# Performance work log

Hardware: AMD Instinct MI355X
Metric: run time of the kernel (lower is better)

Reference implementation:

```python
import jax, jax.numpy as jnp
import numpy as np
import math

B, S, D, H, DFF = 2, 2048, 1024, 16, 4096
DK = D // H
EPS = 1e-5

def layer_norm(x, g, b):
    mu = jnp.mean(x, axis=-1, keepdims=True)
    var = jnp.mean(jnp.square(x - mu), axis=-1, keepdims=True)
    return (x - mu) * jax.lax.rsqrt(var + EPS) * g + b

def setup_inputs() -> dict:
    key = jax.random.key(0)
    ks = jax.random.split(key, 12)
    p = lambda k, shape: (jax.random.normal(k, shape, jnp.float32) * 0.02)
    return {
        "x": jax.random.normal(ks[0], (B, S, D), jnp.float32),
        "mask": jax.random.randint(ks[1], (B, S, S), 0, 2).astype(bool),
        "Wq": p(ks[2], (D, D)), "bq": jnp.zeros((D,), jnp.float32),
        "Wk": p(ks[3], (D, D)), "bk": jnp.zeros((D,), jnp.float32),
        "Wv": p(ks[4], (D, D)), "bv": jnp.zeros((D,), jnp.float32),
        "Wo": p(ks[5], (D, D)), "bo": jnp.zeros((D,), jnp.float32),
        "W1": p(ks[6], (DFF, D)), "b1": jnp.zeros((DFF,), jnp.float32),
        "W2": p(ks[7], (D, DFF)), "b2": jnp.zeros((D,), jnp.float32),
        "g_attn": jnp.ones((D,), jnp.float32), "b_attn": jnp.zeros((D,), jnp.float32),
        "g_ffn": jnp.ones((D,), jnp.float32), "b_ffn": jnp.zeros((D,), jnp.float32),
    }

def reference(x, mask, Wq, bq, Wk, bk, Wv, bv, Wo, bo, W1, b1, W2, b2, g_attn, b_attn, g_ffn, b_ffn):
    orig_dtype = x.dtype
    nx = layer_norm(x, g_attn, b_attn)
    # project and split heads: [B,S,D] -> [B,H,S,DK]
    split = lambda t: t.reshape(B, S, H, DK).transpose(0, 2, 1, 3)
    q = split(nx @ Wq.T + bq)
    k = split(nx @ Wk.T + bk)
    v = split(nx @ Wv.T + bv)
    # explicit fp32 upcast as in the original
    scores = jnp.einsum('bhqd,bhkd->bhqk', q.astype(jnp.float32), k.astype(jnp.float32)) / math.sqrt(DK)
    scores = jnp.where(mask[:, None, :, :], jnp.float32(-10000.0), scores)
    attn = jax.nn.softmax(scores, axis=-1)
    context = jnp.einsum('bhqk,bhkd->bhqd', attn, v.astype(jnp.float32)).astype(orig_dtype)
    context = context.transpose(0, 2, 1, 3).reshape(B, S, D)
    x = x + (context @ Wo.T + bo)
    nx = layer_norm(x, g_ffn, b_ffn)
    h = jax.nn.gelu(nx @ W1.T + b1, approximate=False)  # torch F.gelu default is exact erf
    x = x + (h @ W2.T + b2)
    return x
```

## Files before the change

kernel.cpp:

```cpp
#include <hip/hip_runtime.h>
#include <stdint.h>

#define B_ 2
#define S_ 2048
#define D_ 1024
#define H_ 16
#define DK_ 64
#define DFF_ 4096
#define M_ (B_*S_)

typedef __bf16 bf16x8 __attribute__((ext_vector_type(8)));
typedef float  f32x4  __attribute__((ext_vector_type(4)));

__device__ __forceinline__ unsigned short f2bf(float f) {
    union { float f; unsigned int u; } x; x.f = f;
    unsigned int r = x.u + 0x7FFFu + ((x.u >> 16) & 1u);
    return (unsigned short)(r >> 16);
}
__device__ __forceinline__ float bf2f(unsigned short h) {
    union { unsigned int u; float f; } x; x.u = ((unsigned int)h) << 16;
    return x.f;
}

__device__ __forceinline__ void gl16(const void* g, void* l) {
    __builtin_amdgcn_global_load_lds((const __attribute__((address_space(1))) unsigned int*)g,
                                     (__attribute__((address_space(3))) unsigned int*)l, 16, 0, 0);
}

static constexpr size_t OFS_XC   = 256;
static constexpr size_t OFS_MASK = OFS_XC   + 8388608;
static constexpr size_t OFS_WQKV = OFS_MASK + 8388608;
static constexpr size_t OFS_WO   = OFS_WQKV + 6291456;
static constexpr size_t OFS_W1   = OFS_WO   + 2097152;
static constexpr size_t OFS_W2   = OFS_W1   + 8388608;
static constexpr size_t OFS_BIAS = OFS_W2   + 8388608;
static constexpr size_t OFS_S0   = OFS_BIAS + 53248;
static constexpr size_t OFS_S1   = OFS_S0   + 8388608;
static constexpr size_t OFS_S2   = OFS_S1   + 8388608;
static constexpr size_t OFS_S3   = OFS_S2   + 8388608;
static constexpr size_t OFS_H    = OFS_S3   + 8388608;

#define BOF_QKV 0
#define BOF_O   3072
#define BOF_2   4096
#define BOF_GA  5120
#define BOF_BA  6144
#define BOF_GF  7168
#define BOF_BF  8192
#define BOF_1   9216

__global__ void detect_kernel(const unsigned int* __restrict__ g_attn,
                              const unsigned int* __restrict__ mask,
                              int* __restrict__ flags) {
    const int u = threadIdx.x;
    unsigned int w0 = mask[u], w1 = mask[64 + u];
    bool a32  = (w0 <= 1u) && (w1 <= 1u);
    bool af32 = ((w0 == 0u) || (w0 == 0x3F800000u)) && ((w1 == 0u) || (w1 == 0x3F800000u));
    bool a8 = true;
    #pragma unroll
    for (int j = 0; j < 4; j++)
        a8 = a8 && (((w0 >> (8*j)) & 0xFFu) <= 1u) && (((w1 >> (8*j)) & 0xFFu) <= 1u);
    int all32 = __all(a32), all8 = __all(a8), allf32 = __all(af32);
    if (u == 0) {
        unsigned int g0 = g_attn[0];
        int fm = (g0 == 0x3F800000u) ? 0 : ((g0 == 0x3C003C00u) ? 2 : 1);
        int mm = all32 ? 0 : (all8 ? 1 : (allf32 ? 2 : 3));
        flags[0] = fm; flags[1] = mm;
    }
}

struct BigSrc { const void* s[7]; };

__device__ __forceinline__ void conv4(const void* src, size_t si,
                                      unsigned short* dst, size_t di, int fm) {
    ushort4 ov;
    if (fm == 1) {
        ov = *(const ushort4*)((const unsigned short*)src + si);
    } else if (fm == 0) {
        const float* fp = (const float*)src + si;
        float4 f = *(const float4*)fp;
        ov.x = f2bf(f.x); ov.y = f2bf(f.y); ov.z = f2bf(f.z); ov.w = f2bf(f.w);
    } else {
        const _Float16* hp = (const _Float16*)src + si;
        ov.x = f2bf((float)hp[0]); ov.y = f2bf((float)hp[1]);
        ov.z = f2bf((float)hp[2]); ov.w = f2bf((float)hp[3]);
    }
    *(ushort4*)(dst + di) = ov;
}

__global__ __launch_bounds__(256) void convert_big_kernel(BigSrc srcs, char* ws) {
    const int fm = ((const int*)ws)[0];
    size_t i = ((size_t)blockIdx.x * 256 + threadIdx.x) * 4;
    if (i >= 16777216) return;
    if (i < 4194304) {
        conv4(srcs.s[0], i, (unsigned short*)(ws + OFS_XC), i, fm);
    } else if (i < 7340032) {
        size_t off = i - 4194304;
        int sub = (int)(off >> 20);
        size_t loc = off & 1048575;
        conv4(srcs.s[1 + sub], loc, (unsigned short*)(ws + OFS_WQKV), off, fm);
    } else if (i < 8388608) {
        size_t off = i - 7340032;
        conv4(srcs.s[4], off, (unsigned short*)(ws + OFS_WO), off, fm);
    } else if (i < 12582912) {
        size_t off = i - 8388608;
        conv4(srcs.s[5], off, (unsigned short*)(ws + OFS_W1), off, fm);
    } else {
        size_t off = i - 12582912;
        conv4(srcs.s[6], off, (unsigned short*)(ws + OFS_W2), off, fm);
    }
}

struct SmallSrc { const void* s[10]; };

__global__ __launch_bounds__(256) void convert_small_kernel(SmallSrc srcs, char* ws) {
    int idx = blockIdx.x * 256 + threadIdx.x;
    if (idx >= 13312) return;
    const int fm = ((const int*)ws)[0];
    int seg = idx >> 10; if (seg > 9) seg = 9;
    int loc = idx - seg * 1024;
    const void* s = srcs.s[seg];
    float f;
    if (fm == 1)      f = bf2f(((const unsigned short*)s)[loc]);
    else if (fm == 0) f = ((const float*)s)[loc];
    else              f = (float)((const _Float16*)s)[loc];
    ((float*)(ws + OFS_BIAS))[idx] = f;
}

__global__ __launch_bounds__(256) void mask_bits_kernel(const void* msrc, char* ws) {
    const int mm = ((const int*)ws)[1];
    size_t e = (size_t)blockIdx.x * 256 + threadIdx.x;
    bool p;
    if (mm == 0)      p = ((const int*)msrc)[e] != 0;
    else if (mm == 1) p = ((const unsigned char*)msrc)[e] != 0;
    else if (mm == 2) p = ((const unsigned int*)msrc)[e] != 0;
    else              p = ((const unsigned short*)msrc)[e] != 0;
    unsigned long long bal = __ballot(p);
    if ((threadIdx.x & 63) == 0)
        ((unsigned long long*)(ws + OFS_MASK))[e >> 6] = bal;
}

template<int IN32>
__global__ __launch_bounds__(256) void ln_kernel(const void* __restrict__ xin,
                                                 const float* __restrict__ g,
                                                 const float* __restrict__ b,
                                                 unsigned short* __restrict__ out) {
    const int row = blockIdx.x;
    const int t = threadIdx.x;
    float f0, f1, f2, f3;
    if (IN32) {
        const float* xr = (const float*)xin + (size_t)row * D_;
        float4 xv = *(const float4*)(xr + t * 4);
        f0 = xv.x; f1 = xv.y; f2 = xv.z; f3 = xv.w;
    } else {
        const unsigned short* xr = (const unsigned short*)xin + (size_t)row * D_;
        ushort4 xv = *(const ushort4*)(xr + t * 4);
        f0 = bf2f(xv.x); f1 = bf2f(xv.y); f2 = bf2f(xv.z); f3 = bf2f(xv.w);
    }
    float s = f0 + f1 + f2 + f3;
    float q = f0*f0 + f1*f1 + f2*f2 + f3*f3;
    for (int m = 1; m < 64; m <<= 1) { s += __shfl_xor(s, m); q += __shfl_xor(q, m); }
    __shared__ float red[8];
    __shared__ float mv[2];
    int w = t >> 6, u = t & 63;
    if (u == 0) { red[w*2] = s; red[w*2+1] = q; }
    __syncthreads();
    if (t == 0) {
        float S = red[0] + red[2] + red[4] + red[6];
        float Q = red[1] + red[3] + red[5] + red[7];
        float mu = S * (1.0f / D_);
        float var = Q * (1.0f / D_) - mu * mu;
        mv[0] = mu; mv[1] = rsqrtf(var + 1e-5f);
    }
    __syncthreads();
    float mu = mv[0], r = mv[1];
    int i = t * 4;
    ushort4 ov;
    ov.x = f2bf((f0 - mu) * r * g[i]   + b[i]);
    ov.y = f2bf((f1 - mu) * r * g[i+1] + b[i+1]);
    ov.z = f2bf((f2 - mu) * r * g[i+2] + b[i+2]);
    ov.w = f2bf((f3 - mu) * r * g[i+3] + b[i+3]);
    *(ushort4*)(out + (size_t)row * D_ + i) = ov;
}

template<int EPI>
__global__ __launch_bounds__(256) void gemm_bt_kernel(
    const unsigned short* __restrict__ A,
    const unsigned short* __restrict__ Bm,
    const float* __restrict__ bias,
    void* __restrict__ out,
    float* __restrict__ p1,
    unsigned short* __restrict__ q_out,
    unsigned short* __restrict__ k_out,
    unsigned short* __restrict__ vT_out,
    int M, int N, int K, int Kstride)
{
    __shared__ __attribute__((aligned(16))) unsigned short ldsA[2][4096];
    __shared__ __attribute__((aligned(16))) unsigned short ldsB[2][4096];
    const int t = threadIdx.x;
    const int w = t >> 6, u = t & 63, quad = u >> 4, l15 = u & 15;
    const int bx = blockIdx.x, by = blockIdx.y;
    const int z = (EPI == 5) ? blockIdx.z : 0;

    const int c0 = t, c1 = t + 256;
    const int ar0 = by*128 + ((c0 >> 6) << 4) + (c0 & 15), ak0 = ((c0 >> 4) & 3) * 8;
    const int ar1 = by*128 + ((c1 >> 6) << 4) + (c1 & 15), ak1 = ((c1 >> 4) & 3) * 8;
    const int br0 = bx*128 + ((c0 >> 6) << 4) + (c0 & 15);
    const int br1 = bx*128 + ((c1 >> 6) << 4) + (c1 & 15);
    const size_t kofs = (size_t)z * K;
    const unsigned short* pa0 = A  + (size_t)ar0 * Kstride + kofs + ak0;
    const unsigned short* pa1 = A  + (size_t)ar1 * Kstride + kofs + ak1;
    const unsigned short* pb0 = Bm + (size_t)br0 * Kstride + kofs + ak0;
    const unsigned short* pb1 = Bm + (size_t)br1 * Kstride + kofs + ak1;

    const int cbase0 = (w * 64) * 8;
    const int cbase1 = (256 + w * 64) * 8;

    f32x4 acc[4][4];
    #pragma unroll
    for (int i = 0; i < 4; i++)
        #pragma unroll
        for (int j = 0; j < 4; j++) acc[i][j] = (f32x4){0.f, 0.f, 0.f, 0.f};

    const int mbase = (w >> 1) * 4;
    const int nbase = (w & 1) * 4;

    for (int k0 = 0; k0 < K; k0 += 64) {
        __syncthreads();
        gl16(pa0,      &ldsA[0][cbase0]);
        gl16(pa1,      &ldsA[0][cbase1]);
        gl16(pb0,      &ldsB[0][cbase0]);
        gl16(pb1,      &ldsB[0][cbase1]);
        gl16(pa0 + 32, &ldsA[1][cbase0]);
        gl16(pa1 + 32, &ldsA[1][cbase1]);
        gl16(pb0 + 32, &ldsB[1][cbase0]);
        gl16(pb1 + 32, &ldsB[1][cbase1]);
        pa0 += 64; pa1 += 64; pb0 += 64; pb1 += 64;
        __syncthreads();
        #pragma unroll
        for (int sub = 0; sub < 2; sub++) {
            bf16x8 af[4], bfr[4];
            #pragma unroll
            for (int mt = 0; mt < 4; mt++) af[mt]  = *(const bf16x8*)&ldsA[sub][((mbase+mt)*64 + u) * 8];
            #pragma unroll
            for (int nt = 0; nt < 4; nt++) bfr[nt] = *(const bf16x8*)&ldsB[sub][((nbase+nt)*64 + u) * 8];
            #pragma unroll
            for (int mt = 0; mt < 4; mt++)
                #pragma unroll
                for (int nt = 0; nt < 4; nt++)
                    acc[mt][nt] = __builtin_amdgcn_mfma_f32_16x16x32_bf16(af[mt], bfr[nt], acc[mt][nt], 0, 0, 0);
        }
    }

    #pragma unroll
    for (int mt = 0; mt < 4; mt++) {
        #pragma unroll
        for (int nt = 0; nt < 4; nt++) {
            const int m0 = by*128 + (w >> 1)*64 + mt*16 + quad*4;
            const int n  = bx*128 + (w & 1)*64 + nt*16 + l15;
            float bn = 0.f;
            if constexpr (EPI != 5) bn = bias[n];
            float val[4];
            #pragma unroll
            for (int r = 0; r < 4; r++) val[r] = acc[mt][nt][r] + bn;
            if constexpr (EPI == 1) {
                #pragma unroll
                for (int r = 0; r < 4; r++) {
                    float v = val[r];
                    float ge = 0.5f * v * (1.0f + erff(v * 0.70710678118654752f));
                    ((unsigned short*)out)[(size_t)(m0 + r) * N + n] = f2bf(ge);
                }
            } else if constexpr (EPI == 2) {
                int sel = n >> 10, nn = n & 1023;
                int hh = nn >> 6, dk = nn & 63;
                int bb = m0 >> 11, ss = m0 & 2047;
                if (sel < 2) {
                    unsigned short* dst = sel == 0 ? q_out : k_out;
                    #pragma unroll
                    for (int r = 0; r < 4; r++)
                        dst[(((size_t)bb * H_ + hh) * S_ + ss + r) * DK_ + dk] = f2bf(val[r]);
                } else {
                    ushort4 pk;
                    pk.x = f2bf(val[0]); pk.y = f2bf(val[1]);
                    pk.z = f2bf(val[2]); pk.w = f2bf(val[3]);
                    *(ushort4*)&vT_out[(((size_t)bb * H_ + hh) * DK_ + dk) * S_ + ss] = pk;
                }
            } else {
                float* dst = z ? p1 : (float*)out;
                #pragma unroll
                for (int r = 0; r < 4; r++)
                    dst[(size_t)(m0 + r) * N + n] = val[r];
            }
        }
    }
}

template<int EPI>
__global__ __launch_bounds__(512, 2) void gemm256_kernel(
    const unsigned short* __restrict__ A,
    const unsigned short* __restrict__ Bm,
    const float* __restrict__ bias,
    void* __restrict__ out,
    unsigned short* __restrict__ q_out,
    unsigned short* __restrict__ k_out,
    unsigned short* __restrict__ vT_out,
    int N)
{
    __shared__ __attribute__((aligned(16))) unsigned short sh[2][2][16384];
    const int t = threadIdx.x, w = t >> 6, u = t & 63, quad = u >> 4, l15 = u & 15;
    const int wm = w >> 2, wn = w & 3;
    const int bx = blockIdx.x, by = blockIdx.y;

    const int r1 = t >> 3, cc1 = t & 7, cs1 = cc1 ^ (r1 & 7);
    const unsigned short* srcA = A  + ((size_t)by * 256 + r1) * 1024 + cs1 * 8;
    const unsigned short* srcB = Bm + ((size_t)bx * 256 + r1) * 1024 + cs1 * 8;

    const int rowA = wm * 16 + l15;
    const int rowB = wn * 16 + l15;
    const int cx0 = ((quad    ) ^ (l15 & 7)) * 8;
    const int cx1 = ((quad + 4) ^ (l15 & 7)) * 8;

    f32x4 acc[8][4];
    #pragma unroll
    for (int i = 0; i < 8; i++)
        #pragma unroll
        for (int j = 0; j < 4; j++) acc[i][j] = (f32x4){0.f, 0.f, 0.f, 0.f};

#define STAGE(bufi, mat, half, tile) { \
    const unsigned short* _s = ((mat) ? srcB : srcA) + (size_t)(half) * 131072 + (size_t)(tile) * 64; \
    unsigned short* _d = &sh[bufi][mat][(half) * 8192 + w * 512]; \
    gl16(_s, _d); gl16(_s + 65536, _d + 4096); }

#define LOAD_A(bufi, mh) { \
    const unsigned short* _p = &sh[bufi][0][0]; \
    _Pragma("unroll") \
    for (int f = 0; f < 4; f++) { \
        aF[f][0] = *(const bf16x8*)&_p[((mh) * 128 + f * 32 + rowA) * 64 + cx0]; \
        aF[f][1] = *(const bf16x8*)&_p[((mh) * 128 + f * 32 + rowA) * 64 + cx1]; \
    } }

#define LOAD_B(bufi, nh) { \
    const unsigned short* _p = &sh[bufi][1][0]; \
    _Pragma("unroll") \
    for (int g = 0; g < 2; g++) { \
        bF[nh][g][0] = *(const bf16x8*)&_p[((nh) * 128 + g * 64 + rowB) * 64 + cx0]; \
        bF[nh][g][1] = *(const bf16x8*)&_p[((nh) * 128 + g * 64 + rowB) * 64 + cx1]; \
    } }

#define QUADC(mh, nh) \
    __builtin_amdgcn_s_setprio(1); \
    _Pragma("unroll") \
    for (int ks = 0; ks < 2; ks++) \
        _Pragma("unroll") \
        for (int f = 0; f < 4; f++) \
            _Pragma("unroll") \
            for (int g = 0; g < 2; g++) \
                acc[(mh)*4 + f][(nh)*2 + g] = __builtin_amdgcn_mfma_f32_16x16x32_bf16( \
                    aF[f][ks], bF[nh][g][ks], acc[(mh)*4 + f][(nh)*2 + g], 0, 0, 0); \
    __builtin_amdgcn_s_setprio(0);

#define BARR __builtin_amdgcn_s_barrier()
#define VM6  asm volatile("s_waitcnt vmcnt(6)" ::: "memory")

    STAGE(0, 0, 0, 0);
    STAGE(0, 1, 0, 0);
    STAGE(0, 0, 1, 0);
    STAGE(0, 1, 1, 0);
    STAGE(1, 0, 0, 1);
    STAGE(1, 1, 0, 1);
    STAGE(1, 0, 1, 1);
    VM6;
    BARR;

    bf16x8 aF[4][2];
    bf16x8 bF[2][2][2];

    #pragma unroll 1
    for (int it = 0; it < 8; ++it) {
        const int t1 = 2 * it + 1;
        const int t2 = (it < 7) ? 2 * it + 2 : 15;
        const int t3 = (it < 7) ? 2 * it + 3 : 15;

        LOAD_A(0, 0); LOAD_B(0, 0);
        STAGE(1, 1, 1, t1);
        BARR; QUADC(0, 0); BARR;
        LOAD_B(0, 1);
        STAGE(0, 0, 0, t2);
        BARR; QUADC(0, 1); BARR;
        LOAD_A(0, 1);
        STAGE(0, 1, 0, t2);
        BARR; QUADC(1, 0); BARR;
        STAGE(0, 0, 1, t2);
        VM6;
        BARR; QUADC(1, 1); BARR;
        LOAD_A(1, 0); LOAD_B(1, 0);
        STAGE(0, 1, 1, t2);
        BARR; QUADC(0, 0); BARR;
        LOAD_B(1, 1);
        STAGE(1, 0, 0, t3);
        BARR; QUADC(0, 1); BARR;
        LOAD_A(1, 1);
        STAGE(1, 1, 0, t3);
        BARR; QUADC(1, 0); BARR;
        STAGE(1, 0, 1, t3);
        VM6;
        BARR; QUADC(1, 1); BARR;
    }
    asm volatile("s_waitcnt vmcnt(0)" ::: "memory");

#undef STAGE
#undef LOAD_A
#undef LOAD_B
#undef QUADC
#undef BARR
#undef VM6

    if constexpr (EPI == 1) {
        #pragma unroll
        for (int f = 0; f < 8; f++) {
            #pragma unroll
            for (int g = 0; g < 4; g++) {
                const int m0 = by * 256 + f * 32 + wm * 16 + quad * 4;
                const int n  = bx * 256 + g * 64 + wn * 16 + l15;
                const float bn = bias[n];
                #pragma unroll
                for (int r = 0; r < 4; r++) {
                    float v = acc[f][g][r] + bn;
                    float ge = 0.5f * v * (1.0f + erff(v * 0.70710678118654752f));
                    ((unsigned short*)out)[(size_t)(m0 + r) * N + n] = f2bf(ge);
                }
            }
        }
    } else {
        const int sel = bx >> 2;
        #pragma unroll
        for (int f = 0; f < 8; f++) {
            #pragma unroll
            for (int g = 0; g < 4; g++) {
                const int m0 = by * 256 + f * 32 + wm * 16 + quad * 4;
                const int n  = bx * 256 + g * 64 + wn * 16 + l15;
                const float bn = bias[n];
                const int nn = n & 1023, hh = nn >> 6, dk = nn & 63;
                const int bb = m0 >> 11, ss = m0 & 2047;
                if (sel < 2) {
                    unsigned short* dst = sel == 0 ? q_out : k_out;
                    #pragma unroll
                    for (int r = 0; r < 4; r++)
                        dst[(((size_t)bb * H_ + hh) * S_ + ss + r) * DK_ + dk] = f2bf(acc[f][g][r] + bn);
                } else {
                    ushort4 pk;
                    pk.x = f2bf(acc[f][g][0] + bn); pk.y = f2bf(acc[f][g][1] + bn);
                    pk.z = f2bf(acc[f][g][2] + bn); pk.w = f2bf(acc[f][g][3] + bn);
                    *(ushort4*)&vT_out[(((size_t)bb * H_ + hh) * DK_ + dk) * S_ + ss] = pk;
                }
            }
        }
    }
}

template<int FINAL>
__global__ __launch_bounds__(256) void reduce_kernel(
    const float* __restrict__ p0, const float* __restrict__ p1,
    const float* __restrict__ bias, const void* __restrict__ res,
    void* __restrict__ out, const int* __restrict__ flags)
{
    size_t i = ((size_t)blockIdx.x * 256 + threadIdx.x) * 4;
    int n = (int)(i & 1023);
    float4 a = *(const float4*)(p0 + i);
    float4 b = *(const float4*)(p1 + i);
    const float4 bi = *(const float4*)(bias + n);
    float v0 = a.x + b.x + bi.x, v1 = a.y + b.y + bi.y;
    float v2 = a.z + b.z + bi.z, v3 = a.w + b.w + bi.w;
    if constexpr (FINAL == 0) {
        ushort4 rr = *(const ushort4*)((const unsigned short*)res + i);
        v0 += bf2f(rr.x); v1 += bf2f(rr.y); v2 += bf2f(rr.z); v3 += bf2f(rr.w);
        float4 ov = {v0, v1, v2, v3};
        *(float4*)((float*)out + i) = ov;
    } else {
        float4 rr = *(const float4*)((const float*)res + i);
        v0 += rr.x; v1 += rr.y; v2 += rr.z; v3 += rr.w;
        const int fm = flags[0];
        if (fm == 0) {
            float4 ov = {v0, v1, v2, v3};
            *(float4*)((float*)out + i) = ov;
        } else if (fm == 2) {
            _Float16* op = (_Float16*)out + i;
            op[0] = (_Float16)v0; op[1] = (_Float16)v1;
            op[2] = (_Float16)v2; op[3] = (_Float16)v3;
        } else {
            ushort4 ov;
            ov.x = f2bf(v0); ov.y = f2bf(v1); ov.z = f2bf(v2); ov.w = f2bf(v3);
            *(ushort4*)((unsigned short*)out + i) = ov;
        }
    }
}

__global__ __launch_bounds__(512) void attn_kernel(
    const unsigned short* __restrict__ q,
    const unsigned short* __restrict__ k,
    const unsigned short* __restrict__ vT,
    const unsigned long long* __restrict__ mb,
    unsigned short* __restrict__ ctx)
{
    const int blk = blockIdx.x;
    const int xcd = blk & 7;
    const int slot = blk >> 3;
    const int qt = slot & 15;
    const int pg = slot >> 4;
    const int p  = xcd + 8 * pg;
    const int h = p & 15, b = p >> 4;
    const int bh = b * H_ + h;

    const int t = threadIdx.x, w = t >> 6, u = t & 63, quad = u >> 4, l15 = u & 15;

    __shared__ __attribute__((aligned(16))) unsigned short Kt[512 * 8];
    __shared__ __attribute__((aligned(16))) unsigned short Vt[512 * 8];
    __shared__ __attribute__((aligned(16))) unsigned short Pw[8][16 * 72];

    const size_t base = (size_t)bh * S_ * DK_;
    const int qr0 = qt * 128 + w * 16;

    bf16x8 aq[2];
    #pragma unroll
    for (int hf = 0; hf < 2; hf++)
        aq[hf] = *(const bf16x8*)(q + base + (size_t)(qr0 + l15) * DK_ + hf*32 + quad*8);

    const int sr = t >> 3, sc = (t & 7) ^ (sr & 7);
    const unsigned short* kp = k  + base + (size_t)sr * DK_ + sc * 8;
    const unsigned short* vp = vT + base + (size_t)sr * S_  + sc * 8;
    unsigned short* lk = &Kt[(w * 64) * 8];
    unsigned short* lv = &Vt[(w * 64) * 8];

    f32x4 o[4];
    #pragma unroll
    for (int nt = 0; nt < 4; nt++) o[nt] = (f32x4){0.f, 0.f, 0.f, 0.f};
    float ls[4] = {0.f, 0.f, 0.f, 0.f};
    const float C = 0.125f * 1.4426950408889634f;

    for (int kt = 0; kt < S_ / 64; kt++) {
        unsigned long long m64[4];
        #pragma unroll
        for (int r = 0; r < 4; r++)
            m64[r] = mb[((size_t)b * S_ + qr0 + quad*4 + r) * 32 + kt];

        __syncthreads();
        gl16(kp, lk);
        gl16(vp, lv);
        kp += 64 * DK_;
        vp += 64;
        __syncthreads();

        f32x4 s4[4];
        #pragma unroll
        for (int nt = 0; nt < 4; nt++) s4[nt] = (f32x4){0.f, 0.f, 0.f, 0.f};
        #pragma unroll
        for (int nt = 0; nt < 4; nt++) {
            int rr = nt * 16 + l15;
            #pragma unroll
            for (int hf = 0; hf < 2; hf++) {
                int cc = (hf * 4 + quad) ^ (rr & 7);
                bf16x8 bk = *(const bf16x8*)&Kt[(rr * 8 + cc) * 8];
                s4[nt] = __builtin_amdgcn_mfma_f32_16x16x32_bf16(aq[hf], bk, s4[nt], 0, 0, 0);
            }
        }

        #pragma unroll
        for (int r = 0; r < 4; r++) {
            unsigned int lo = (unsigned int)m64[r], hi = (unsigned int)(m64[r] >> 32);
            #pragma unroll
            for (int nt = 0; nt < 4; nt++) {
                unsigned int word = (nt & 2) ? hi : lo;
                unsigned int bit = (word >> ((nt & 1) * 16 + l15)) & 1u;
                float arg = bit ? -20000.0f : s4[nt][r] * C;
                float e = exp2f(arg);
                ls[r] += e;
                Pw[w][(quad * 4 + r) * 72 + nt * 16 + l15] = f2bf(e);
            }
        }

        #pragma unroll
        for (int ks = 0; ks < 2; ks++) {
            bf16x8 ap = *(const bf16x8*)&Pw[w][l15 * 72 + ks * 32 + quad * 8];
            #pragma unroll
            for (int nt = 0; nt < 4; nt++) {
                int rr = nt * 16 + l15;
                int cc = (ks * 4 + quad) ^ (rr & 7);
                bf16x8 bv = *(const bf16x8*)&Vt[(rr * 8 + cc) * 8];
                o[nt] = __builtin_amdgcn_mfma_f32_16x16x32_bf16(ap, bv, o[nt], 0, 0, 0);
            }
        }
    }

    #pragma unroll
    for (int r = 0; r < 4; r++) {
        float l = ls[r];
        l += __shfl_xor(l, 1); l += __shfl_xor(l, 2);
        l += __shfl_xor(l, 4); l += __shfl_xor(l, 8);
        float inv = 1.0f / l;
        int qg = qr0 + quad * 4 + r;
        #pragma unroll
        for (int nt = 0; nt < 4; nt++)
            ctx[((size_t)b * S_ + qg) * D_ + h * DK_ + nt * 16 + l15] = f2bf(o[nt][r] * inv);
    }
}

extern "C" void kernel_launch(void* const* d_in, const int* in_sizes, int n_in,
                              void* d_out, int out_size, void* d_ws, size_t ws_size,
                              hipStream_t stream) {
    char* ws = (char*)d_ws;

    detect_kernel<<<1, 64, 0, stream>>>((const unsigned int*)d_in[14],
                                        (const unsigned int*)d_in[1], (int*)ws);

    BigSrc bs; bs.s[0] = d_in[0]; bs.s[1] = d_in[2]; bs.s[2] = d_in[4];
    bs.s[3] = d_in[6]; bs.s[4] = d_in[8]; bs.s[5] = d_in[10]; bs.s[6] = d_in[12];
    convert_big_kernel<<<16384, 256, 0, stream>>>(bs, ws);

    SmallSrc ss;
    ss.s[0] = d_in[3];  ss.s[1] = d_in[5];  ss.s[2] = d_in[7];  ss.s[3] = d_in[9];
    ss.s[4] = d_in[13]; ss.s[5] = d_in[14]; ss.s[6] = d_in[15]; ss.s[7] = d_in[16];
    ss.s[8] = d_in[17]; ss.s[9] = d_in[11];
    convert_small_kernel<<<52, 256, 0, stream>>>(ss, ws);

    mask_bits_kernel<<<32768, 256, 0, stream>>>(d_in[1], ws);

    const unsigned short* xc  = (const unsigned short*)(ws + OFS_XC);
    const unsigned short* wqk = (const unsigned short*)(ws + OFS_WQKV);
    const unsigned short* wo  = (const unsigned short*)(ws + OFS_WO);
    const unsigned short* w1  = (const unsigned short*)(ws + OFS_W1);
    const unsigned short* w2  = (const unsigned short*)(ws + OFS_W2);
    float* biasf = (float*)(ws + OFS_BIAS);
    unsigned short* nx1 = (unsigned short*)(ws + OFS_S0);
    unsigned short* ctx = (unsigned short*)(ws + OFS_S0);
    unsigned short* nx2 = (unsigned short*)(ws + OFS_S0);
    unsigned short* qb  = (unsigned short*)(ws + OFS_S1);
    unsigned short* kb  = (unsigned short*)(ws + OFS_S2);
    unsigned short* vTb = (unsigned short*)(ws + OFS_S3);
    float*          x2f = (float*)(ws + OFS_S2);
    unsigned short* hb  = (unsigned short*)(ws + OFS_H);
    float* opart0 = (float*)(ws + OFS_H);
    float* opart1 = (float*)(ws + OFS_H + 16777216);
    float* fpart0 = (float*)(ws + OFS_XC);
    float* fpart1 = (float*)(ws + OFS_S0);
    const unsigned long long* mbits = (const unsigned long long*)(ws + OFS_MASK);
    const int* flags = (const int*)ws;

    ln_kernel<0><<<4096, 256, 0, stream>>>(xc, biasf + BOF_GA, biasf + BOF_BA, nx1);

    gemm256_kernel<2><<<dim3(12, 16), 512, 0, stream>>>(
        nx1, wqk, biasf + BOF_QKV, nullptr, qb, kb, vTb, 3072);

    attn_kernel<<<512, 512, 0, stream>>>(qb, kb, vTb, mbits, ctx);

    gemm_bt_kernel<5><<<dim3(8, 32, 2), 256, 0, stream>>>(
        ctx, wo, nullptr, opart0, opart1, nullptr, nullptr, nullptr, M_, 1024, 512, 1024);
    reduce_kernel<0><<<4096, 256, 0, stream>>>(
        opart0, opart1, biasf + BOF_O, xc, x2f, flags);

    ln_kernel<1><<<4096, 256, 0, stream>>>(x2f, biasf + BOF_GF, biasf + BOF_BF, nx2);

    gemm256_kernel<1><<<dim3(16, 16), 512, 0, stream>>>(
        nx2, w1, biasf + BOF_1, hb, nullptr, nullptr, nullptr, 4096);

    gemm_bt_kernel<5><<<dim3(8, 32, 2), 256, 0, stream>>>(
        hb, w2, nullptr, fpart0, fpart1, nullptr, nullptr, nullptr, M_, 1024, 2048, 4096);
    reduce_kernel<1><<<4096, 256, 0, stream>>>(
        fpart0, fpart1, biasf + BOF_2, x2f, d_out, flags);
}
```

Before: 463.1 us.

## Run FFN down-projection on 256-tile GEMM with 4-way split-K

Generalizes the 256x256 GEMM kernel to any K and row stride and adds a split-K epilogue that writes fp32 partials. The FFN down projection (K=4096) now runs on this larger-tile kernel with a 4-way K split and a new 4-input reduce kernel, replacing the smaller-tile 2-way split GEMM. The goal is better MFMA efficiency and data reuse on the largest GEMM. In exchange it writes and reads twice as much partial-sum traffic, and one partial buffer falls back to the weight region or the output buffer depending on workspace size.

```diff
diff --git a/kernel.cpp b/kernel.cpp
--- a/kernel.cpp
+++ b/kernel.cpp
@@ -48,6 +48,8 @@
 #define BOF_GF  7168
 #define BOF_BF  8192
 #define BOF_1   9216
+
+struct Parts { float* p[4]; };
 
 __global__ void detect_kernel(const unsigned int* __restrict__ g_attn,
                               const unsigned int* __restrict__ mask,
@@ -304,16 +306,21 @@
     unsigned short* __restrict__ q_out,
     unsigned short* __restrict__ k_out,
     unsigned short* __restrict__ vT_out,
-    int N)
+    Parts parts,
+    int N, int K, int Kstride)
 {
     __shared__ __attribute__((aligned(16))) unsigned short sh[2][2][16384];
     const int t = threadIdx.x, w = t >> 6, u = t & 63, quad = u >> 4, l15 = u & 15;
     const int wm = w >> 2, wn = w & 3;
     const int bx = blockIdx.x, by = blockIdx.y;
+    const int z = (EPI == 5) ? blockIdx.z : 0;
+    const size_t kofs = (size_t)z * K;
 
     const int r1 = t >> 3, cc1 = t & 7, cs1 = cc1 ^ (r1 & 7);
-    const unsigned short* srcA = A  + ((size_t)by * 256 + r1) * 1024 + cs1 * 8;
-    const unsigned short* srcB = Bm + ((size_t)bx * 256 + r1) * 1024 + cs1 * 8;
+    const unsigned short* srcA = A  + ((size_t)by * 256 + r1) * Kstride + kofs + cs1 * 8;
+    const unsigned short* srcB = Bm + ((size_t)bx * 256 + r1) * Kstride + kofs + cs1 * 8;
+    const size_t halfstep = 128 * (size_t)Kstride;
+    const size_t rowstep64 = 64 * (size_t)Kstride;
 
     const int rowA = wm * 16 + l15;
     const int rowB = wn * 16 + l15;
@@ -327,9 +334,9 @@
         for (int j = 0; j < 4; j++) acc[i][j] = (f32x4){0.f, 0.f, 0.f, 0.f};
 
 #define STAGE(bufi, mat, half, tile) { \
-    const unsigned short* _s = ((mat) ? srcB : srcA) + (size_t)(half) * 131072 + (size_t)(tile) * 64; \
+    const unsigned short* _s = ((mat) ? srcB : srcA) + (size_t)(half) * halfstep + (size_t)(tile) * 64; \
     unsigned short* _d = &sh[bufi][mat][(half) * 8192 + w * 512]; \
-    gl16(_s, _d); gl16(_s + 65536, _d + 4096); }
+    gl16(_s, _d); gl16(_s + rowstep64, _d + 4096); }
 
 #define LOAD_A(bufi, mh) { \
     const unsigned short* _p = &sh[bufi][0][0]; \
@@ -375,11 +382,14 @@
     bf16x8 aF[4][2];
     bf16x8 bF[2][2][2];
 
+    const int nIt = K >> 7;
+    const int lastT = (K >> 6) - 1;
+
     #pragma unroll 1
-    for (int it = 0; it < 8; ++it) {
+    for (int it = 0; it < nIt; ++it) {
         const int t1 = 2 * it + 1;
-        const int t2 = (it < 7) ? 2 * it + 2 : 15;
-        const int t3 = (it < 7) ? 2 * it + 3 : 15;
+        const int t2 = (it < nIt - 1) ? 2 * it + 2 : lastT;
+        const int t3 = (it < nIt - 1) ? 2 * it + 3 : lastT;
 
         LOAD_A(0, 0); LOAD_B(0, 0);
         STAGE(1, 1, 1, t1);
@@ -431,7 +441,7 @@
                 }
             }
         }
-    } else {
+    } else if constexpr (EPI == 2) {
         const int sel = bx >> 2;
         #pragma unroll
         for (int f = 0; f < 8; f++) {
@@ -453,6 +463,19 @@
                     pk.z = f2bf(acc[f][g][2] + bn); pk.w = f2bf(acc[f][g][3] + bn);
                     *(ushort4*)&vT_out[(((size_t)bb * H_ + hh) * DK_ + dk) * S_ + ss] = pk;
                 }
+            }
+        }
+    } else {
+        float* dst = parts.p[z];
+        #pragma unroll
+        for (int f = 0; f < 8; f++) {
+            #pragma unroll
+            for (int g = 0; g < 4; g++) {
+                const int m0 = by * 256 + f * 32 + wm * 16 + quad * 4;
+                const int n  = bx * 256 + g * 64 + wn * 16 + l15;
+                #pragma unroll
+                for (int r = 0; r < 4; r++)
+                    dst[(size_t)(m0 + r) * N + n] = acc[f][g][r];
             }
         }
     }
@@ -495,6 +518,37 @@
     }
 }
 
+__global__ __launch_bounds__(256) void reduce4_kernel(
+    Parts parts, const float* __restrict__ bias, const float* __restrict__ res,
+    void* __restrict__ out, const int* __restrict__ flags)
+{
+    size_t i = ((size_t)blockIdx.x * 256 + threadIdx.x) * 4;
+    int n = (int)(i & 1023);
+    float4 a = *(const float4*)(parts.p[0] + i);
+    float4 b = *(const float4*)(parts.p[1] + i);
+    float4 c = *(const float4*)(parts.p[2] + i);
+    float4 d = *(const float4*)(parts.p[3] + i);
+    const float4 bi = *(const float4*)(bias + n);
+    float4 rr = *(const float4*)(res + i);
+    float v0 = (a.x + b.x) + (c.x + d.x) + bi.x + rr.x;
+    float v1 = (a.y + b.y) + (c.y + d.y) + bi.y + rr.y;
+    float v2 = (a.z + b.z) + (c.z + d.z) + bi.z + rr.z;
+    float v3 = (a.w + b.w) + (c.w + d.w) + bi.w + rr.w;
+    const int fm = flags[0];
+    if (fm == 0) {
+        float4 ov = {v0, v1, v2, v3};
+        *(float4*)((float*)out + i) = ov;
+    } else if (fm == 2) {
+        _Float16* op = (_Float16*)out + i;
+        op[0] = (_Float16)v0; op[1] = (_Float16)v1;
+        op[2] = (_Float16)v2; op[3] = (_Float16)v3;
+    } else {
+        ushort4 ov;
+        ov.x = f2bf(v0); ov.y = f2bf(v1); ov.z = f2bf(v2); ov.w = f2bf(v3);
+        *(ushort4*)((unsigned short*)out + i) = ov;
+    }
+}
+
 __global__ __launch_bounds__(512) void attn_kernel(
     const unsigned short* __restrict__ q,
     const unsigned short* __restrict__ k,
@@ -640,15 +694,15 @@
     unsigned short* hb  = (unsigned short*)(ws + OFS_H);
     float* opart0 = (float*)(ws + OFS_H);
     float* opart1 = (float*)(ws + OFS_H + 16777216);
-    float* fpart0 = (float*)(ws + OFS_XC);
-    float* fpart1 = (float*)(ws + OFS_S0);
     const unsigned long long* mbits = (const unsigned long long*)(ws + OFS_MASK);
     const int* flags = (const int*)ws;
 
+    Parts noparts = {};
+
     ln_kernel<0><<<4096, 256, 0, stream>>>(xc, biasf + BOF_GA, biasf + BOF_BA, nx1);
 
     gemm256_kernel<2><<<dim3(12, 16), 512, 0, stream>>>(
-        nx1, wqk, biasf + BOF_QKV, nullptr, qb, kb, vTb, 3072);
+        nx1, wqk, biasf + BOF_QKV, nullptr, qb, kb, vTb, noparts, 3072, 1024, 1024);
 
     attn_kernel<<<512, 512, 0, stream>>>(qb, kb, vTb, mbits, ctx);
 
@@ -660,10 +714,27 @@
     ln_kernel<1><<<4096, 256, 0, stream>>>(x2f, biasf + BOF_GF, biasf + BOF_BF, nx2);
 
     gemm256_kernel<1><<<dim3(16, 16), 512, 0, stream>>>(
-        nx2, w1, biasf + BOF_1, hb, nullptr, nullptr, nullptr, 4096);
-
-    gemm_bt_kernel<5><<<dim3(8, 32, 2), 256, 0, stream>>>(
-        hb, w2, nullptr, fpart0, fpart1, nullptr, nullptr, nullptr, M_, 1024, 2048, 4096);
-    reduce_kernel<1><<<4096, 256, 0, stream>>>(
-        fpart0, fpart1, biasf + BOF_2, x2f, d_out, flags);
-}
+        nx2, w1, biasf + BOF_1, hb, nullptr, nullptr, nullptr, noparts, 4096, 1024, 1024);
+
+    float* fp3 = nullptr;
+    if (ws_size >= OFS_H + 33554432 + 16777216)      fp3 = (float*)(ws + OFS_H + 33554432);
+    else if ((size_t)out_size >= 16777216)           fp3 = (float*)d_out;
+
+    if (fp3) {
+        Parts pp;
+        pp.p[0] = (float*)(ws + OFS_XC);
+        pp.p[1] = (float*)(ws + OFS_S0);
+        pp.p[2] = (float*)(ws + OFS_WQKV);
+        pp.p[3] = fp3;
+        gemm256_kernel<5><<<dim3(4, 16, 4), 512, 0, stream>>>(
+            hb, w2, nullptr, nullptr, nullptr, nullptr, nullptr, pp, 1024, 1024, 4096);
+        reduce4_kernel<<<4096, 256, 0, stream>>>(pp, biasf + BOF_2, x2f, d_out, flags);
+    } else {
+        float* fpart0 = (float*)(ws + OFS_XC);
+        float* fpart1 = (float*)(ws + OFS_S0);
+        gemm_bt_kernel<5><<<dim3(8, 32, 2), 256, 0, stream>>>(
+            hb, w2, nullptr, fpart0, fpart1, nullptr, nullptr, nullptr, M_, 1024, 2048, 4096);
+        reduce_kernel<1><<<4096, 256, 0, stream>>>(
+            fpart0, fpart1, biasf + BOF_2, x2f, d_out, flags);
+    }
+}
```

Result: faster. 431.9 us (-6.7%).
